# Performance work log

Hardware: AMD Instinct MI355X
Metric: run time of the kernel (lower is better)

The kernel has to match this reference:

```python
import jax, jax.numpy as jnp
import numpy as np

N_NODES = 8192
N_EDGES = 65536
NB = 10            # number_of_basis
MID = 32           # middle_layer_size
MAX_R = 10.0       # max_radius
NZ, NM = 48, 16    # z / mol embedding sizes -> 64x0e node input
IN_S = NZ + NM     # 64 scalars
H_S, H_V = 32, 8   # hidden irreps 32x0e + 8x1o (dim 56)
O_S = 16           # output irreps 16x0e
W0N = IN_S * H_S + IN_S * H_V                                  # 2560
W1N = H_S*H_S + H_V*H_S + H_S*H_V + H_V*H_V + H_V*H_V          # 1664
W2N = H_S*O_S + H_V*O_S                                        # 640
H_DIM = H_S + 3 * H_V                                          # 56


def _fcnet(e, W1, W2):
    # e3nn FullyConnectedNet([NB, MID, numel], silu): fan-in normalized linears
    h = jax.nn.silu(e @ W1 / np.sqrt(W1.shape[0]))
    return h @ W2 / np.sqrt(W2.shape[0])


def _ln(x, g, b):
    m = jnp.mean(x, -1, keepdims=True)
    v = jnp.var(x, -1, keepdims=True)
    return (x - m) * jax.lax.rsqrt(v + 1e-5) * g + b


def _sus(t):
    # smooth compact-support bump helper: exp(-1/t) for t>0 else 0
    return jnp.where(t > 0, jnp.exp(-1.0 / jnp.where(t > 0, t, 1.0)), 0.0)


def _forward(pos, Ez, Em,
             b0_W1, b0_W2, b0_g, b0_b,
             b1_W1, b1_W2, b1_g, b1_b,
             b2_W1, b2_W2, b2_g, b2_b,
             z, mol_id, edge_src, edge_dst):
    N = pos.shape[0]
    E = edge_src.shape[0]
    avg = E / N  # avg_num_neighbors (static)

    # node embedding: 64x0e
    x = jnp.concatenate([Ez[z], Em[mol_id]], axis=-1)          # [N, 64]

    vec = pos[edge_dst] - pos[edge_src]                        # [E, 3]
    length = jnp.linalg.norm(vec, axis=1)                      # [E]

    # soft_one_hot_linspace(basis='smooth_finite', cutoff=True) * sqrt(NB)
    vals = jnp.linspace(0.0, MAX_R, NB + 2)[1:-1]
    step = MAX_R / (NB + 1)
    u = (length[:, None] - vals) / step
    emb = (1.14136 * np.exp(2.0)) * _sus(u + 1.0) * _sus(1.0 - u)
    emb = emb * np.sqrt(NB)                                    # [E, NB]

    # spherical harmonics lmax=1, normalize=True, 'component' norm
    nrm = vec / jnp.maximum(length, 1e-9)[:, None]
    sh_v = np.sqrt(3.0) * nrm                                  # [E, 3]  (l=1; l=0 comp == 1)

    # ---- interaction block 0: 64x0e -> 32x0e + 8x1o ----
    w = _fcnet(emb, b0_W1, b0_W2)                              # [E, 2560]
    w00 = w[:, :IN_S * H_S].reshape(E, IN_S, H_S)
    w01 = w[:, IN_S * H_S:].reshape(E, IN_S, H_V)
    xe = x[edge_src]                                           # [E, 64]
    es = jnp.einsum('eu,euw->ew', xe, w00) / np.sqrt(IN_S)
    ev = jnp.einsum('eu,euw,ei->ewi', xe, w01, sh_v) / np.sqrt(IN_S)
    msg = jnp.concatenate([es, ev.reshape(E, 3 * H_V)], -1)    # [E, 56]
    x = _ln(jax.ops.segment_sum(msg, edge_dst, num_segments=N) / np.sqrt(avg), b0_g, b0_b)

    # ---- interaction block 1: 32x0e+8x1o -> 32x0e+8x1o ----
    w = _fcnet(emb, b1_W1, b1_W2)                              # [E, 1664]
    o = 0
    w_ss  = w[:, o:o + H_S*H_S].reshape(E, H_S, H_S); o += H_S*H_S
    w_vvs = w[:, o:o + H_V*H_S].reshape(E, H_V, H_S); o += H_V*H_S
    w_sv  = w[:, o:o + H_S*H_V].reshape(E, H_S, H_V); o += H_S*H_V
    w_vs  = w[:, o:o + H_V*H_V].reshape(E, H_V, H_V); o += H_V*H_V
    w_vvv = w[:, o:o + H_V*H_V].reshape(E, H_V, H_V)
    xs = x[:, :H_S][edge_src]                                  # [E, 32]
    xv = x[:, H_S:].reshape(N, H_V, 3)[edge_src]               # [E, 8, 3]
    dot = jnp.einsum('eui,ei->eu', xv, sh_v) / np.sqrt(3.0)    # 1o x 1o -> 0e CG
    crs = jnp.cross(xv, sh_v[:, None, :]) / np.sqrt(2.0)       # 1o x 1o -> 1o CG
    es = (jnp.einsum('eu,euw->ew', xs, w_ss) / np.sqrt(H_S)
          + jnp.einsum('eu,euw->ew', dot, w_vvs) / np.sqrt(H_V)) / np.sqrt(2.0)
    ev = (jnp.einsum('eu,euw,ei->ewi', xs, w_sv, sh_v) / np.sqrt(H_S)
          + jnp.einsum('eui,euw->ewi', xv, w_vs) / np.sqrt(H_V)
          + jnp.einsum('eui,euw->ewi', crs, w_vvv) / np.sqrt(H_V)) / np.sqrt(3.0)
    msg = jnp.concatenate([es, ev.reshape(E, 3 * H_V)], -1)
    x = _ln(jax.ops.segment_sum(msg, edge_dst, num_segments=N) / np.sqrt(avg), b1_g, b1_b)

    # ---- interaction block 2: 32x0e+8x1o -> 16x0e ----
    w = _fcnet(emb, b2_W1, b2_W2)                              # [E, 640]
    w_ss  = w[:, :H_S * O_S].reshape(E, H_S, O_S)
    w_vvs = w[:, H_S * O_S:].reshape(E, H_V, O_S)
    xs = x[:, :H_S][edge_src]
    xv = x[:, H_S:].reshape(N, H_V, 3)[edge_src]
    dot = jnp.einsum('eui,ei->eu', xv, sh_v) / np.sqrt(3.0)
    es = (jnp.einsum('eu,euw->ew', xs, w_ss) / np.sqrt(H_S)
          + jnp.einsum('eu,euw->ew', dot, w_vvs) / np.sqrt(H_V)) / np.sqrt(2.0)
    x = _ln(jax.ops.segment_sum(es, edge_dst, num_segments=N) / np.sqrt(avg), b2_g, b2_b)
    return x                                                   # [N, 16]


def setup_inputs():
    key = jax.random.key(0)
    ks = jax.random.split(key, 16)
    edge_src = jax.random.randint(ks[3], (N_EDGES,), 0, N_NODES)
    # exclude self-loops (radius_graph never returns them)
    edge_dst = (edge_src + 1 + jax.random.randint(ks[4], (N_EDGES,), 0, N_NODES - 1)) % N_NODES
    return {
        'pos': jax.random.uniform(ks[0], (N_NODES, 3), jnp.float32) * 8.0,
        'z': jax.random.randint(ks[1], (N_NODES,), 0, 100),
        'mol_id': jax.random.randint(ks[2], (N_NODES,), 0, 2),
        'edge_src': edge_src,
        'edge_dst': edge_dst,
        'Ez': jax.random.normal(ks[5], (100, NZ), jnp.float32),
        'Em': jax.random.normal(ks[6], (2, NM), jnp.float32),
        'b0_W1': jax.random.normal(ks[7], (NB, MID), jnp.float32),
        'b0_W2': jax.random.normal(ks[8], (MID, W0N), jnp.float32),
        'b0_g': jnp.ones((H_DIM,), jnp.float32),
        'b0_b': jnp.zeros((H_DIM,), jnp.float32),
        'b1_W1': jax.random.normal(ks[9], (NB, MID), jnp.float32),
        'b1_W2': jax.random.normal(ks[10], (MID, W1N), jnp.float32),
        'b1_g': jnp.ones((H_DIM,), jnp.float32),
        'b1_b': jnp.zeros((H_DIM,), jnp.float32),
        'b2_W1': jax.random.normal(ks[11], (NB, MID), jnp.float32),
        'b2_W2': jax.random.normal(ks[12], (MID, W2N), jnp.float32),
        'b2_g': jnp.ones((O_S,), jnp.float32),
        'b2_b': jnp.zeros((O_S,), jnp.float32),
    }


def reference(pos, z, mol_id, edge_src, edge_dst, Ez, Em,
              b0_W1, b0_W2, b0_g, b0_b,
              b1_W1, b1_W2, b1_g, b1_b,
              b2_W1, b2_W2, b2_g, b2_b):
    return _forward(pos, Ez, Em,
                    b0_W1, b0_W2, b0_g, b0_b,
                    b1_W1, b1_W2, b1_g, b1_b,
                    b2_W1, b2_W2, b2_g, b2_b,
                    z, mol_id, edge_src, edge_dst)
```

## Files before the change

### kernel.cpp

```cpp
#include <hip/hip_runtime.h>

#define NNODES 8192
#define NEDGES 65536

#define K_PACK   0.02209708691f
#define K_P1SV   0.01804219593f
#define K_VVS    0.04419417382f
#define K_VS     0.03608439182f
#define K_VVV    0.02551551815f
#define K_DOT    0.57735026919f
#define K_PRELN  0.35355339059f
#define C_EMB    8.4335730689f

typedef unsigned int uint32;
typedef unsigned short ushort16;
typedef __attribute__((ext_vector_type(8))) short short8;
typedef __attribute__((ext_vector_type(4))) float floatx4;

__device__ __forceinline__ float siluf(float x) { return x / (1.0f + __expf(-x)); }
__device__ __forceinline__ float susf(float t) { return t > 0.0f ? __expf(-1.0f / t) : 0.0f; }
__device__ __forceinline__ ushort16 f2bf(float f) {
  uint32 u = __float_as_uint(f);
  return (ushort16)((u + 0x7fffu + ((u >> 16) & 1u)) >> 16);
}
__device__ __forceinline__ float bflo(uint32 v) { return __uint_as_float(v << 16); }
__device__ __forceinline__ float bfhi(uint32 v) { return __uint_as_float(v & 0xffff0000u); }

__device__ __forceinline__ void mlp32(const float* __restrict__ W, const float emb[10],
                                      float* __restrict__ H) {
#pragma unroll
  for (int m = 0; m < 32; ++m) {
    float t = 0.f;
#pragma unroll
    for (int k = 0; k < 10; ++k) t += emb[k] * W[k * 32 + m];
    H[m] = siluf(t);
  }
}

__global__ __launch_bounds__(256) void k_prep(
    const float* __restrict__ pos, const int* __restrict__ z, const int* __restrict__ mol,
    const int* __restrict__ esrc, const int* __restrict__ edst,
    const float* __restrict__ Ez, const float* __restrict__ Em,
    const float* __restrict__ W10, const float* __restrict__ W11, const float* __restrict__ W12,
    const float* __restrict__ W20, const float* __restrict__ W21, const float* __restrict__ W22,
    int* __restrict__ combo, ushort16* __restrict__ X0cb, float* __restrict__ sh,
    float* __restrict__ h0, float* __restrict__ h1, float* __restrict__ h2,
    ushort16* __restrict__ h1b, ushort16* __restrict__ h2b,
    ushort16* __restrict__ Bp0, ushort16* __restrict__ Bp1, ushort16* __restrict__ Bp2,
    ushort16* __restrict__ Bpw1, ushort16* __restrict__ Bpw2, int* __restrict__ deg) {
  int idx = blockIdx.x * 256 + threadIdx.x;
  if (idx < NEDGES) {
    int e = idx;
    int s = esrc[e], d = edst[e];
    atomicAdd(&deg[d], 1);
    float vx = pos[d * 3 + 0] - pos[s * 3 + 0];
    float vy = pos[d * 3 + 1] - pos[s * 3 + 1];
    float vz = pos[d * 3 + 2] - pos[s * 3 + 2];
    float len = sqrtf(vx * vx + vy * vy + vz * vz);
    float inv = 1.7320508076f / fmaxf(len, 1e-9f);
    sh[e * 3 + 0] = vx * inv; sh[e * 3 + 1] = vy * inv; sh[e * 3 + 2] = vz * inv;
    float emb[10];
#pragma unroll
    for (int k = 0; k < 10; ++k) {
      float u = len * 1.1f - (float)(k + 1);
      emb[k] = C_EMB * susf(u + 1.0f) * susf(1.0f - u);
    }
    float H[32];
    mlp32(W10, emb, H);
#pragma unroll
    for (int m = 0; m < 32; ++m) h0[(size_t)e * 32 + m] = H[m];
    mlp32(W11, emb, H);
#pragma unroll
    for (int m = 0; m < 32; ++m) {
      h1[(size_t)e * 32 + m] = H[m];
      h1b[(size_t)e * 32 + m] = f2bf(H[m]);
    }
    mlp32(W12, emb, H);
#pragma unroll
    for (int m = 0; m < 32; ++m) {
      h2[(size_t)e * 32 + m] = H[m];
      h2b[(size_t)e * 32 + m] = f2bf(H[m]);
    }
    return;
  }
  idx -= NEDGES;
  if (idx < NNODES) { combo[idx] = z[idx] * 2 + mol[idx]; return; }
  idx -= NNODES;
  if (idx < 16384) {
    int c = idx >> 6, j = idx & 63;
    float v = 0.f;
    if (c < 200) {
      int zz = c >> 1, mm = c & 1;
      v = (j < 48) ? Ez[zz * 48 + j] : Em[mm * 16 + (j - 48)];
    }
    X0cb[idx] = f2bf(v);
    return;
  }
  idx -= 16384;
  if (idx < 81920) {
    int tile = idx >> 10; int r = idx & 1023;
    int kh = r >> 9; int rr = r & 511;
    int lane = rr >> 3, j = rr & 7;
    int k = kh * 32 + (lane >> 4) * 8 + j;
    int n = tile * 16 + (lane & 15);
    int c = n >> 5, m = n & 31;
    int col = (c < 32) ? (k * 32 + c) : (2048 + k * 8 + (c - 32));
    Bp0[idx] = f2bf(W20[m * 2560 + col] * K_PACK);
    return;
  }
  idx -= 81920;
  if (idx < 40960) {
    int tile = idx >> 9; int rr = idx & 511;
    int lane = rr >> 3, j = rr & 7;
    int k = (lane >> 4) * 8 + j;
    int n = tile * 16 + (lane & 15);
    int c = n >> 5, m = n & 31;
    float v = (c < 32) ? W21[m * 1664 + k * 32 + c] * K_PACK
                       : W21[m * 1664 + 1280 + k * 8 + (c - 32)] * K_P1SV;
    Bp1[idx] = f2bf(v);
    return;
  }
  idx -= 40960;
  if (idx < 16384) {
    int tile = idx >> 9; int rr = idx & 511;
    int lane = rr >> 3, j = rr & 7;
    int k = (lane >> 4) * 8 + j;
    int n = tile * 16 + (lane & 15);
    int c = n >> 5, m = n & 31;
    Bp2[idx] = f2bf(W22[m * 640 + k * 16 + c] * K_PACK);
    return;
  }
  idx -= 16384;
  if (idx < 12288) {
    int tile = idx >> 9; int rr = idx & 511;
    int lane = rr >> 3, j = rr & 7;
    int m = (lane >> 4) * 8 + j;
    int c = tile * 16 + (lane & 15);
    float v;
    if (c < 256) {
      int u = c >> 5, w = c & 31;
      v = W21[m * 1664 + 1024 + u * 32 + w] * K_VVS;
    } else {
      int r2 = c - 256; int t = r2 & 1; int l2 = r2 >> 1;
      int u = l2 >> 3, vv = l2 & 7;
      v = (t == 0) ? W21[m * 1664 + 1536 + u * 8 + vv] * K_VS
                   : W21[m * 1664 + 1600 + u * 8 + vv] * K_VVV;
    }
    Bpw1[idx] = f2bf(v);
    return;
  }
  idx -= 12288;
  {
    int tile = idx >> 9; int rr = idx & 511;
    int lane = rr >> 3, j = rr & 7;
    int m = (lane >> 4) * 8 + j;
    int c = tile * 16 + (lane & 15);
    int t = c & 1; int l2 = c >> 1;
    int u = l2 >> 3, wh = l2 & 7;
    Bpw2[idx] = f2bf(W22[m * 640 + 512 + u * 16 + wh * 2 + t] * K_VVS);
  }
}

__global__ __launch_bounds__(256) void k_scan(const int* __restrict__ deg,
                                              int* __restrict__ rowptr) {
  __shared__ int sums[256];
  int t = threadIdx.x;
  int base = t * 32;
  int local[32];
  int s = 0;
#pragma unroll
  for (int i = 0; i < 32; ++i) { local[i] = s; s += deg[base + i]; }
  sums[t] = s;
  __syncthreads();
  for (int off = 1; off < 256; off <<= 1) {
    int v = (t >= off) ? sums[t - off] : 0;
    __syncthreads();
    sums[t] += v;
    __syncthreads();
  }
  int prev = (t == 0) ? 0 : sums[t - 1];
#pragma unroll
  for (int i = 0; i < 32; ++i) rowptr[base + i] = prev + local[i];
  if (t == 255) rowptr[NNODES] = sums[255];
}

__global__ __launch_bounds__(256) void k_fill(const int* __restrict__ edst,
                                              const int* __restrict__ rowptr,
                                              int* __restrict__ fill, int* __restrict__ eidx) {
  int e = blockIdx.x * 256 + threadIdx.x;
  if (e >= NEDGES) return;
  int d = edst[e];
  int p = atomicAdd(&fill[d], 1);
  eidx[rowptr[d] + p] = e;
}

__global__ __launch_bounds__(256) void k_gemm_mfma(
    const ushort16* __restrict__ A, const ushort16* __restrict__ Bp, ushort16* __restrict__ C,
    int N, int K) {
  int wave = threadIdx.x >> 6, lane = threadIdx.x & 63;
  int m0 = blockIdx.x * 64 + wave * 16;
  int n0 = blockIdx.y * 64;
  int row = lane & 15, q = lane >> 4;
  int nkh = K >> 5;
  floatx4 acc[4];
  floatx4 zero = {0.f, 0.f, 0.f, 0.f};
#pragma unroll
  for (int t = 0; t < 4; ++t) acc[t] = zero;
  for (int kh = 0; kh < nkh; ++kh) {
    short8 a = *reinterpret_cast<const short8*>(A + (size_t)(m0 + row) * K + kh * 32 + q * 8);
#pragma unroll
    for (int t = 0; t < 4; ++t) {
      int T = (n0 >> 4) + t;
      short8 b = *reinterpret_cast<const short8*>(Bp + ((size_t)T * nkh + kh) * 512 + lane * 8);
      acc[t] = __builtin_amdgcn_mfma_f32_16x16x32_bf16(a, b, acc[t], 0, 0, 0);
    }
  }
  int colb = n0 + row;
#pragma unroll
  for (int t = 0; t < 4; ++t)
#pragma unroll
    for (int r = 0; r < 4; ++r)
      C[(size_t)(m0 + q * 4 + r) * N + colb + t * 16] = f2bf(acc[t][r]);
}

__global__ __launch_bounds__(256) void k_msg0(
    const int* __restrict__ rowmap, const int* __restrict__ esrc,
    const float* __restrict__ sh, const float* __restrict__ h,
    const ushort16* __restrict__ Pb, float* __restrict__ msg) {
  int e = __builtin_amdgcn_readfirstlane(blockIdx.x * 4 + (threadIdx.x >> 6));
  int lane = threadIdx.x & 63;
  int s = esrc[e];
  int row = rowmap[s];
  float sh0 = sh[e * 3 + 0], sh1 = sh[e * 3 + 1], sh2 = sh[e * 3 + 2];
  int c; float mult;
  if (lane < 32) { c = lane; mult = 1.0f; }
  else if (lane < 56) {
    int l = lane - 32; int v = l / 3; int i = l - v * 3;
    c = 32 + v;
    mult = (i == 0) ? sh0 : (i == 1 ? sh1 : sh2);
  } else { c = 0; mult = 0.0f; }
  const float* hp = h + (size_t)e * 32;
  const uint4* Pp = reinterpret_cast<const uint4*>(Pb + (size_t)row * 1280 + c * 32);
  float a = 0.f;
#pragma unroll
  for (int qq = 0; qq < 4; ++qq) {
    uint4 pv = Pp[qq];
    const float* hq = hp + qq * 8;
    a += bflo(pv.x) * hq[0] + bfhi(pv.x) * hq[1];
    a += bflo(pv.y) * hq[2] + bfhi(pv.y) * hq[3];
    a += bflo(pv.z) * hq[4] + bfhi(pv.z) * hq[5];
    a += bflo(pv.w) * hq[6] + bfhi(pv.w) * hq[7];
  }
  if (lane < 56) msg[(size_t)e * 56 + lane] = a * mult;
}

__global__ __launch_bounds__(256) void k_msg1(
    const int* __restrict__ esrc, const float* __restrict__ sh, const float* __restrict__ h,
    const ushort16* __restrict__ Pb, const float* __restrict__ xv,
    const ushort16* __restrict__ Wedge, float* __restrict__ msg) {
  __shared__ float vbuf[4][56];
  int w = threadIdx.x >> 6;
  int e = __builtin_amdgcn_readfirstlane(blockIdx.x * 4 + w);
  int lane = threadIdx.x & 63;
  int s = esrc[e];
  float sh0 = sh[e * 3 + 0], sh1 = sh[e * 3 + 1], sh2 = sh[e * 3 + 2];
  int u = lane >> 3;
  const float* xvp = xv + (size_t)s * 24 + u * 3;
  float x0 = xvp[0], x1 = xvp[1], x2 = xvp[2];
  float du = K_DOT * (x0 * sh0 + x1 * sh1 + x2 * sh2);
  float cr0 = x1 * sh2 - x2 * sh1;
  float cr1 = x2 * sh0 - x0 * sh2;
  float cr2 = x0 * sh1 - x1 * sh0;
  const ushort16* wp = Wedge + (size_t)e * 384;
  uint2 wv = *reinterpret_cast<const uint2*>(wp + lane * 4);
  uint32 wsv = *reinterpret_cast<const uint32*>(wp + 256 + lane * 2);
  float b0 = du * bflo(wv.x), b1 = du * bfhi(wv.x);
  float b2 = du * bflo(wv.y), b3 = du * bfhi(wv.y);
  float avs = bflo(wsv), avv = bfhi(wsv);
  float e0v = x0 * avs + cr0 * avv;
  float e1v = x1 * avs + cr1 * avv;
  float e2v = x2 * avs + cr2 * avv;
#pragma unroll
  for (int off = 8; off < 64; off <<= 1) {
    b0 += __shfl_xor(b0, off, 64); b1 += __shfl_xor(b1, off, 64);
    b2 += __shfl_xor(b2, off, 64); b3 += __shfl_xor(b3, off, 64);
    e0v += __shfl_xor(e0v, off, 64); e1v += __shfl_xor(e1v, off, 64);
    e2v += __shfl_xor(e2v, off, 64);
  }
  if (lane < 8) {
    vbuf[w][lane * 4 + 0] = b0; vbuf[w][lane * 4 + 1] = b1;
    vbuf[w][lane * 4 + 2] = b2; vbuf[w][lane * 4 + 3] = b3;
    vbuf[w][32 + lane * 3 + 0] = e0v;
    vbuf[w][32 + lane * 3 + 1] = e1v;
    vbuf[w][32 + lane * 3 + 2] = e2v;
  }
  int c; float mult;
  if (lane < 32) { c = lane; mult = 1.0f; }
  else if (lane < 56) {
    int l = lane - 32; int v = l / 3; int i = l - v * 3;
    c = 32 + v;
    mult = (i == 0) ? sh0 : (i == 1 ? sh1 : sh2);
  } else { c = 0; mult = 0.0f; }
  const float* hp = h + (size_t)e * 32;
  const uint4* Pp = reinterpret_cast<const uint4*>(Pb + (size_t)s * 1280 + c * 32);
  float a = 0.f;
#pragma unroll
  for (int qq = 0; qq < 4; ++qq) {
    uint4 pv = Pp[qq];
    const float* hq = hp + qq * 8;
    a += bflo(pv.x) * hq[0] + bfhi(pv.x) * hq[1];
    a += bflo(pv.y) * hq[2] + bfhi(pv.y) * hq[3];
    a += bflo(pv.z) * hq[4] + bfhi(pv.z) * hq[5];
    a += bflo(pv.w) * hq[6] + bfhi(pv.w) * hq[7];
  }
  __syncthreads();
  if (lane < 56) msg[(size_t)e * 56 + lane] = a * mult + vbuf[w][lane];
}

__global__ __launch_bounds__(256) void k_msg2(
    const int* __restrict__ esrc, const float* __restrict__ sh, const float* __restrict__ h,
    const ushort16* __restrict__ Pb, const float* __restrict__ xv,
    const ushort16* __restrict__ Wedge, float* __restrict__ msg) {
  __shared__ float vbuf[4][16];
  int w = threadIdx.x >> 6;
  int e = __builtin_amdgcn_readfirstlane(blockIdx.x * 4 + w);
  int lane = threadIdx.x & 63;
  int s = esrc[e];
  float sh0 = sh[e * 3 + 0], sh1 = sh[e * 3 + 1], sh2 = sh[e * 3 + 2];
  int u = lane >> 3;
  const float* xvp = xv + (size_t)s * 24 + u * 3;
  float du = K_DOT * (xvp[0] * sh0 + xvp[1] * sh1 + xvp[2] * sh2);
  uint32 w2 = *reinterpret_cast<const uint32*>(Wedge + (size_t)e * 128 + lane * 2);
  float c0 = du * bflo(w2), c1 = du * bfhi(w2);
#pragma unroll
  for (int off = 8; off < 64; off <<= 1) {
    c0 += __shfl_xor(c0, off, 64); c1 += __shfl_xor(c1, off, 64);
  }
  if (lane < 8) { vbuf[w][lane * 2 + 0] = c0; vbuf[w][lane * 2 + 1] = c1; }
  int q = lane >> 4, wc = lane & 15;
  const float* hq = h + (size_t)e * 32 + q * 8;
  uint4 pv = reinterpret_cast<const uint4*>(Pb + (size_t)s * 512 + wc * 32)[q];
  float a = bflo(pv.x) * hq[0] + bfhi(pv.x) * hq[1]
          + bflo(pv.y) * hq[2] + bfhi(pv.y) * hq[3]
          + bflo(pv.z) * hq[4] + bfhi(pv.z) * hq[5]
          + bflo(pv.w) * hq[6] + bfhi(pv.w) * hq[7];
  a += __shfl_xor(a, 16, 64);
  a += __shfl_xor(a, 32, 64);
  __syncthreads();
  if (lane < 16) msg[(size_t)e * 16 + lane] = a + vbuf[w][lane];
}

__global__ __launch_bounds__(256) void k_gather_ln(
    const int* __restrict__ rowptr, const int* __restrict__ eidx,
    const float* __restrict__ msg, int D,
    const float* __restrict__ g, const float* __restrict__ b,
    ushort16* __restrict__ xsb, float* __restrict__ xvf, float* __restrict__ outf) {
  int n = __builtin_amdgcn_readfirstlane(blockIdx.x * 4 + (threadIdx.x >> 6));
  int lane = threadIdx.x & 63;
  int r0 = rowptr[n], r1 = rowptr[n + 1];
  float v = 0.f;
  for (int j = r0; j < r1; ++j) {
    int e = eidx[j];
    if (lane < D) v += msg[(size_t)e * D + lane];
  }
  v *= K_PRELN;
  if (lane >= D) v = 0.f;
  float sm = v, sq = v * v;
#pragma unroll
  for (int off = 32; off > 0; off >>= 1) {
    sm += __shfl_xor(sm, off, 64);
    sq += __shfl_xor(sq, off, 64);
  }
  float invD = 1.0f / (float)D;
  float mean = sm * invD;
  float var = sq * invD - mean * mean;
  float rs = rsqrtf(var + 1e-5f);
  float r = (v - mean) * rs * g[lane < D ? lane : 0] + b[lane < D ? lane : 0];
  if (outf) {
    if (lane < D) outf[(size_t)n * D + lane] = r;
  } else {
    if (lane < 32) xsb[(size_t)n * 32 + lane] = f2bf(r);
    else if (lane < 56) xvf[(size_t)n * 24 + lane - 32] = r;
  }
}

extern "C" void kernel_launch(void* const* d_in, const int* in_sizes, int n_in,
                              void* d_out, int out_size, void* d_ws, size_t ws_size,
                              hipStream_t stream) {
  const float* pos = (const float*)d_in[0];
  const int* z = (const int*)d_in[1];
  const int* mol = (const int*)d_in[2];
  const int* esrc = (const int*)d_in[3];
  const int* edst = (const int*)d_in[4];
  const float* Ez = (const float*)d_in[5];
  const float* Em = (const float*)d_in[6];
  const float* b0W1 = (const float*)d_in[7];
  const float* b0W2 = (const float*)d_in[8];
  const float* b0g = (const float*)d_in[9];
  const float* b0b = (const float*)d_in[10];
  const float* b1W1 = (const float*)d_in[11];
  const float* b1W2 = (const float*)d_in[12];
  const float* b1g = (const float*)d_in[13];
  const float* b1b = (const float*)d_in[14];
  const float* b2W1 = (const float*)d_in[15];
  const float* b2W2 = (const float*)d_in[16];
  const float* b2g = (const float*)d_in[17];
  const float* b2b = (const float*)d_in[18];
  float* out = (float*)d_out;

  float* ws = (float*)d_ws;
  size_t o = 0;
  int* combo = (int*)(ws + o); o += NNODES;
  int* deg = (int*)(ws + o); o += NNODES;
  int* fill = (int*)(ws + o); o += NNODES;
  int* rowptr = (int*)(ws + o); o += NNODES + 8;
  int* eidx = (int*)(ws + o); o += NEDGES;
  ushort16* X0cb = (ushort16*)(ws + o); o += 8192;
  ushort16* xs1b = (ushort16*)(ws + o); o += 131072;
  float* xv1 = ws + o; o += (size_t)NNODES * 24;
  float* h0 = ws + o; o += (size_t)NEDGES * 32;
  float* h1 = ws + o; o += (size_t)NEDGES * 32;
  float* h2 = ws + o; o += (size_t)NEDGES * 32;
  float* shb = ws + o; o += (size_t)NEDGES * 3;
  ushort16* Bp0 = (ushort16*)(ws + o); o += 40960;
  ushort16* Bp1 = (ushort16*)(ws + o); o += 20480;
  ushort16* Bp2 = (ushort16*)(ws + o); o += 8192;
  ushort16* Bpw1 = (ushort16*)(ws + o); o += 6144;
  ushort16* Bpw2 = (ushort16*)(ws + o); o += 2048;
  ushort16* h1b = (ushort16*)(ws + o); o += (size_t)NEDGES * 16;
  ushort16* h2b = (ushort16*)(ws + o); o += (size_t)NEDGES * 16;
  ushort16* Wedge1 = (ushort16*)(ws + o); o += (size_t)NEDGES * 192;
  ushort16* P12 = (ushort16*)(ws + o); o += (size_t)NNODES * 640;
  float* msg56 = ws + o; o += (size_t)NEDGES * 56;

  ushort16* P0c = P12;
  ushort16* xs2b = xs1b;
  float* xv2 = xv1;
  ushort16* Wedge2 = Wedge1;
  float* msg16 = msg56;

  hipMemsetAsync(deg, 0, 2 * NNODES * sizeof(int), stream);

  k_prep<<<960, 256, 0, stream>>>(pos, z, mol, esrc, edst, Ez, Em,
                                  b0W1, b1W1, b2W1, b0W2, b1W2, b2W2,
                                  combo, X0cb, shb, h0, h1, h2, h1b, h2b,
                                  Bp0, Bp1, Bp2, Bpw1, Bpw2, deg);
  k_scan<<<1, 256, 0, stream>>>(deg, rowptr);
  k_fill<<<256, 256, 0, stream>>>(edst, rowptr, fill, eidx);

  k_gemm_mfma<<<dim3(4, 20), 256, 0, stream>>>(X0cb, Bp0, P0c, 1280, 64);
  k_gemm_mfma<<<dim3(1024, 6), 256, 0, stream>>>(h1b, Bpw1, Wedge1, 384, 32);
  k_msg0<<<16384, 256, 0, stream>>>(combo, esrc, shb, h0, P0c, msg56);
  k_gather_ln<<<2048, 256, 0, stream>>>(rowptr, eidx, msg56, 56, b0g, b0b, xs1b, xv1, nullptr);

  k_gemm_mfma<<<dim3(128, 20), 256, 0, stream>>>(xs1b, Bp1, P12, 1280, 32);
  k_msg1<<<16384, 256, 0, stream>>>(esrc, shb, h1, P12, xv1, Wedge1, msg56);
  k_gather_ln<<<2048, 256, 0, stream>>>(rowptr, eidx, msg56, 56, b1g, b1b, xs2b, xv2, nullptr);

  k_gemm_mfma<<<dim3(1024, 2), 256, 0, stream>>>(h2b, Bpw2, Wedge2, 128, 32);
  k_gemm_mfma<<<dim3(128, 8), 256, 0, stream>>>(xs2b, Bp2, P12, 512, 32);
  k_msg2<<<16384, 256, 0, stream>>>(esrc, shb, h2, P12, xv2, Wedge2, msg16);
  k_gather_ln<<<2048, 256, 0, stream>>>(rowptr, eidx, msg16, 16, b2g, b2b, nullptr, nullptr, out);
}
```

Measured before the change: 254.2 us.

## Store edge MLP hidden as bf16 only and batch three GEMMs into one launch

The edge radial-MLP hidden activations are now written only as packed bf16, and the fp32 copies go away. The message kernels read them with 16-byte vector loads, which cuts k_prep store traffic and halves the hidden-vector reads in msg0/msg1/msg2. Three independent GEMMs (the Wedge1 and Wedge2 edge-weight GEMMs and the P0 node GEMM) are merged into a single launch with a block-index dispatcher. Wedge2 gets its own buffer so it can be computed early. The cost is extra workspace and a small precision loss from using bf16 hidden values in the fp32-P dot products.

Result: no change. 256.5 us (+0.9%).

```diff
diff --git a/kernel.cpp b/kernel.cpp
--- a/kernel.cpp
+++ b/kernel.cpp
@@ -44,8 +44,7 @@
     const float* __restrict__ W10, const float* __restrict__ W11, const float* __restrict__ W12,
     const float* __restrict__ W20, const float* __restrict__ W21, const float* __restrict__ W22,
     int* __restrict__ combo, ushort16* __restrict__ X0cb, float* __restrict__ sh,
-    float* __restrict__ h0, float* __restrict__ h1, float* __restrict__ h2,
-    ushort16* __restrict__ h1b, ushort16* __restrict__ h2b,
+    ushort16* __restrict__ h0b, ushort16* __restrict__ h1b, ushort16* __restrict__ h2b,
     ushort16* __restrict__ Bp0, ushort16* __restrict__ Bp1, ushort16* __restrict__ Bp2,
     ushort16* __restrict__ Bpw1, ushort16* __restrict__ Bpw2, int* __restrict__ deg) {
   int idx = blockIdx.x * 256 + threadIdx.x;
@@ -66,21 +65,22 @@
       emb[k] = C_EMB * susf(u + 1.0f) * susf(1.0f - u);
     }
     float H[32];
+    uint32* hp;
     mlp32(W10, emb, H);
-#pragma unroll
-    for (int m = 0; m < 32; ++m) h0[(size_t)e * 32 + m] = H[m];
+    hp = (uint32*)(h0b + (size_t)e * 32);
+#pragma unroll
+    for (int m = 0; m < 16; ++m)
+      hp[m] = (uint32)f2bf(H[2 * m]) | ((uint32)f2bf(H[2 * m + 1]) << 16);
     mlp32(W11, emb, H);
-#pragma unroll
-    for (int m = 0; m < 32; ++m) {
-      h1[(size_t)e * 32 + m] = H[m];
-      h1b[(size_t)e * 32 + m] = f2bf(H[m]);
-    }
+    hp = (uint32*)(h1b + (size_t)e * 32);
+#pragma unroll
+    for (int m = 0; m < 16; ++m)
+      hp[m] = (uint32)f2bf(H[2 * m]) | ((uint32)f2bf(H[2 * m + 1]) << 16);
     mlp32(W12, emb, H);
-#pragma unroll
-    for (int m = 0; m < 32; ++m) {
-      h2[(size_t)e * 32 + m] = H[m];
-      h2b[(size_t)e * 32 + m] = f2bf(H[m]);
-    }
+    hp = (uint32*)(h2b + (size_t)e * 32);
+#pragma unroll
+    for (int m = 0; m < 16; ++m)
+      hp[m] = (uint32)f2bf(H[2 * m]) | ((uint32)f2bf(H[2 * m + 1]) << 16);
     return;
   }
   idx -= NEDGES;
@@ -194,12 +194,11 @@
   eidx[rowptr[d] + p] = e;
 }
 
-__global__ __launch_bounds__(256) void k_gemm_mfma(
+__device__ __forceinline__ void gemm_tile(
     const ushort16* __restrict__ A, const ushort16* __restrict__ Bp, ushort16* __restrict__ C,
-    int N, int K) {
-  int wave = threadIdx.x >> 6, lane = threadIdx.x & 63;
-  int m0 = blockIdx.x * 64 + wave * 16;
-  int n0 = blockIdx.y * 64;
+    int N, int K, int bx, int by, int wave, int lane) {
+  int m0 = bx * 64 + wave * 16;
+  int n0 = by * 64;
   int row = lane & 15, q = lane >> 4;
   int nkh = K >> 5;
   floatx4 acc[4];
@@ -223,9 +222,35 @@
       C[(size_t)(m0 + q * 4 + r) * N + colb + t * 16] = f2bf(acc[t][r]);
 }
 
+__global__ __launch_bounds__(256) void k_gemm_mfma(
+    const ushort16* __restrict__ A, const ushort16* __restrict__ Bp, ushort16* __restrict__ C,
+    int N, int K) {
+  gemm_tile(A, Bp, C, N, K, blockIdx.x, blockIdx.y, threadIdx.x >> 6, threadIdx.x & 63);
+}
+
+__global__ __launch_bounds__(256) void k_gemm3(
+    const ushort16* __restrict__ A0, const ushort16* __restrict__ B0, ushort16* __restrict__ C0,
+    int N0, int K0, int nbx0, int nb0,
+    const ushort16* __restrict__ A1, const ushort16* __restrict__ B1, ushort16* __restrict__ C1,
+    int N1, int K1, int nbx1, int nb1,
+    const ushort16* __restrict__ A2, const ushort16* __restrict__ B2, ushort16* __restrict__ C2,
+    int N2, int K2, int nbx2) {
+  int b = blockIdx.x;
+  int wave = threadIdx.x >> 6, lane = threadIdx.x & 63;
+  if (b < nb0) {
+    gemm_tile(A0, B0, C0, N0, K0, b % nbx0, b / nbx0, wave, lane);
+  } else if (b < nb0 + nb1) {
+    b -= nb0;
+    gemm_tile(A1, B1, C1, N1, K1, b % nbx1, b / nbx1, wave, lane);
+  } else {
+    b -= nb0 + nb1;
+    gemm_tile(A2, B2, C2, N2, K2, b % nbx2, b / nbx2, wave, lane);
+  }
+}
+
 __global__ __launch_bounds__(256) void k_msg0(
     const int* __restrict__ rowmap, const int* __restrict__ esrc,
-    const float* __restrict__ sh, const float* __restrict__ h,
+    const float* __restrict__ sh, const ushort16* __restrict__ hb,
     const ushort16* __restrict__ Pb, float* __restrict__ msg) {
   int e = __builtin_amdgcn_readfirstlane(blockIdx.x * 4 + (threadIdx.x >> 6));
   int lane = threadIdx.x & 63;
@@ -239,23 +264,23 @@
     c = 32 + v;
     mult = (i == 0) ? sh0 : (i == 1 ? sh1 : sh2);
   } else { c = 0; mult = 0.0f; }
-  const float* hp = h + (size_t)e * 32;
+  const uint4* Hp = reinterpret_cast<const uint4*>(hb + (size_t)e * 32);
   const uint4* Pp = reinterpret_cast<const uint4*>(Pb + (size_t)row * 1280 + c * 32);
   float a = 0.f;
 #pragma unroll
   for (int qq = 0; qq < 4; ++qq) {
     uint4 pv = Pp[qq];
-    const float* hq = hp + qq * 8;
-    a += bflo(pv.x) * hq[0] + bfhi(pv.x) * hq[1];
-    a += bflo(pv.y) * hq[2] + bfhi(pv.y) * hq[3];
-    a += bflo(pv.z) * hq[4] + bfhi(pv.z) * hq[5];
-    a += bflo(pv.w) * hq[6] + bfhi(pv.w) * hq[7];
+    uint4 hv = Hp[qq];
+    a += bflo(pv.x) * bflo(hv.x) + bfhi(pv.x) * bfhi(hv.x);
+    a += bflo(pv.y) * bflo(hv.y) + bfhi(pv.y) * bfhi(hv.y);
+    a += bflo(pv.z) * bflo(hv.z) + bfhi(pv.z) * bfhi(hv.z);
+    a += bflo(pv.w) * bflo(hv.w) + bfhi(pv.w) * bfhi(hv.w);
   }
   if (lane < 56) msg[(size_t)e * 56 + lane] = a * mult;
 }
 
 __global__ __launch_bounds__(256) void k_msg1(
-    const int* __restrict__ esrc, const float* __restrict__ sh, const float* __restrict__ h,
+    const int* __restrict__ esrc, const float* __restrict__ sh, const ushort16* __restrict__ hb,
     const ushort16* __restrict__ Pb, const float* __restrict__ xv,
     const ushort16* __restrict__ Wedge, float* __restrict__ msg) {
   __shared__ float vbuf[4][56];
@@ -301,24 +326,24 @@
     c = 32 + v;
     mult = (i == 0) ? sh0 : (i == 1 ? sh1 : sh2);
   } else { c = 0; mult = 0.0f; }
-  const float* hp = h + (size_t)e * 32;
+  const uint4* Hp = reinterpret_cast<const uint4*>(hb + (size_t)e * 32);
   const uint4* Pp = reinterpret_cast<const uint4*>(Pb + (size_t)s * 1280 + c * 32);
   float a = 0.f;
 #pragma unroll
   for (int qq = 0; qq < 4; ++qq) {
     uint4 pv = Pp[qq];
-    const float* hq = hp + qq * 8;
-    a += bflo(pv.x) * hq[0] + bfhi(pv.x) * hq[1];
-    a += bflo(pv.y) * hq[2] + bfhi(pv.y) * hq[3];
-    a += bflo(pv.z) * hq[4] + bfhi(pv.z) * hq[5];
-    a += bflo(pv.w) * hq[6] + bfhi(pv.w) * hq[7];
+    uint4 hv = Hp[qq];
+    a += bflo(pv.x) * bflo(hv.x) + bfhi(pv.x) * bfhi(hv.x);
+    a += bflo(pv.y) * bflo(hv.y) + bfhi(pv.y) * bfhi(hv.y);
+    a += bflo(pv.z) * bflo(hv.z) + bfhi(pv.z) * bfhi(hv.z);
+    a += bflo(pv.w) * bflo(hv.w) + bfhi(pv.w) * bfhi(hv.w);
   }
   __syncthreads();
   if (lane < 56) msg[(size_t)e * 56 + lane] = a * mult + vbuf[w][lane];
 }
 
 __global__ __launch_bounds__(256) void k_msg2(
-    const int* __restrict__ esrc, const float* __restrict__ sh, const float* __restrict__ h,
+    const int* __restrict__ esrc, const float* __restrict__ sh, const ushort16* __restrict__ hb,
     const ushort16* __restrict__ Pb, const float* __restrict__ xv,
     const ushort16* __restrict__ Wedge, float* __restrict__ msg) {
   __shared__ float vbuf[4][16];
@@ -338,12 +363,12 @@
   }
   if (lane < 8) { vbuf[w][lane * 2 + 0] = c0; vbuf[w][lane * 2 + 1] = c1; }
   int q = lane >> 4, wc = lane & 15;
-  const float* hq = h + (size_t)e * 32 + q * 8;
+  uint4 hv = reinterpret_cast<const uint4*>(hb + (size_t)e * 32)[q];
   uint4 pv = reinterpret_cast<const uint4*>(Pb + (size_t)s * 512 + wc * 32)[q];
-  float a = bflo(pv.x) * hq[0] + bfhi(pv.x) * hq[1]
-          + bflo(pv.y) * hq[2] + bfhi(pv.y) * hq[3]
-          + bflo(pv.z) * hq[4] + bfhi(pv.z) * hq[5]
-          + bflo(pv.w) * hq[6] + bfhi(pv.w) * hq[7];
+  float a = bflo(pv.x) * bflo(hv.x) + bfhi(pv.x) * bfhi(hv.x)
+          + bflo(pv.y) * bflo(hv.y) + bfhi(pv.y) * bfhi(hv.y)
+          + bflo(pv.z) * bflo(hv.z) + bfhi(pv.z) * bfhi(hv.z)
+          + bflo(pv.w) * bflo(hv.w) + bfhi(pv.w) * bfhi(hv.w);
   a += __shfl_xor(a, 16, 64);
   a += __shfl_xor(a, 32, 64);
   __syncthreads();
@@ -418,47 +443,46 @@
   ushort16* X0cb = (ushort16*)(ws + o); o += 8192;
   ushort16* xs1b = (ushort16*)(ws + o); o += 131072;
   float* xv1 = ws + o; o += (size_t)NNODES * 24;
-  float* h0 = ws + o; o += (size_t)NEDGES * 32;
-  float* h1 = ws + o; o += (size_t)NEDGES * 32;
-  float* h2 = ws + o; o += (size_t)NEDGES * 32;
+  ushort16* h0b = (ushort16*)(ws + o); o += (size_t)NEDGES * 16;
+  ushort16* h1b = (ushort16*)(ws + o); o += (size_t)NEDGES * 16;
+  ushort16* h2b = (ushort16*)(ws + o); o += (size_t)NEDGES * 16;
   float* shb = ws + o; o += (size_t)NEDGES * 3;
   ushort16* Bp0 = (ushort16*)(ws + o); o += 40960;
   ushort16* Bp1 = (ushort16*)(ws + o); o += 20480;
   ushort16* Bp2 = (ushort16*)(ws + o); o += 8192;
   ushort16* Bpw1 = (ushort16*)(ws + o); o += 6144;
   ushort16* Bpw2 = (ushort16*)(ws + o); o += 2048;
-  ushort16* h1b = (ushort16*)(ws + o); o += (size_t)NEDGES * 16;
-  ushort16* h2b = (ushort16*)(ws + o); o += (size_t)NEDGES * 16;
   ushort16* Wedge1 = (ushort16*)(ws + o); o += (size_t)NEDGES * 192;
+  ushort16* Wedge2 = (ushort16*)(ws + o); o += (size_t)NEDGES * 64;
   ushort16* P12 = (ushort16*)(ws + o); o += (size_t)NNODES * 640;
   float* msg56 = ws + o; o += (size_t)NEDGES * 56;
 
   ushort16* P0c = P12;
   ushort16* xs2b = xs1b;
   float* xv2 = xv1;
-  ushort16* Wedge2 = Wedge1;
   float* msg16 = msg56;
 
   hipMemsetAsync(deg, 0, 2 * NNODES * sizeof(int), stream);
 
   k_prep<<<960, 256, 0, stream>>>(pos, z, mol, esrc, edst, Ez, Em,
                                   b0W1, b1W1, b2W1, b0W2, b1W2, b2W2,
-                                  combo, X0cb, shb, h0, h1, h2, h1b, h2b,
+                                  combo, X0cb, shb, h0b, h1b, h2b,
                                   Bp0, Bp1, Bp2, Bpw1, Bpw2, deg);
   k_scan<<<1, 256, 0, stream>>>(deg, rowptr);
   k_fill<<<256, 256, 0, stream>>>(edst, rowptr, fill, eidx);
 
-  k_gemm_mfma<<<dim3(4, 20), 256, 0, stream>>>(X0cb, Bp0, P0c, 1280, 64);
-  k_gemm_mfma<<<dim3(1024, 6), 256, 0, stream>>>(h1b, Bpw1, Wedge1, 384, 32);
-  k_msg0<<<16384, 256, 0, stream>>>(combo, esrc, shb, h0, P0c, msg56);
+  k_gemm3<<<8272, 256, 0, stream>>>(h1b, Bpw1, Wedge1, 384, 32, 1024, 6144,
+                                    h2b, Bpw2, Wedge2, 128, 32, 1024, 2048,
+                                    X0cb, Bp0, P0c, 1280, 64, 4);
+
+  k_msg0<<<16384, 256, 0, stream>>>(combo, esrc, shb, h0b, P0c, msg56);
   k_gather_ln<<<2048, 256, 0, stream>>>(rowptr, eidx, msg56, 56, b0g, b0b, xs1b, xv1, nullptr);
 
   k_gemm_mfma<<<dim3(128, 20), 256, 0, stream>>>(xs1b, Bp1, P12, 1280, 32);
-  k_msg1<<<16384, 256, 0, stream>>>(esrc, shb, h1, P12, xv1, Wedge1, msg56);
+  k_msg1<<<16384, 256, 0, stream>>>(esrc, shb, h1b, P12, xv1, Wedge1, msg56);
   k_gather_ln<<<2048, 256, 0, stream>>>(rowptr, eidx, msg56, 56, b1g, b1b, xs2b, xv2, nullptr);
 
-  k_gemm_mfma<<<dim3(1024, 2), 256, 0, stream>>>(h2b, Bpw2, Wedge2, 128, 32);
   k_gemm_mfma<<<dim3(128, 8), 256, 0, stream>>>(xs2b, Bp2, P12, 512, 32);
-  k_msg2<<<16384, 256, 0, stream>>>(esrc, shb, h2, P12, xv2, Wedge2, msg16);
+  k_msg2<<<16384, 256, 0, stream>>>(esrc, shb, h2b, P12, xv2, Wedge2, msg16);
   k_gather_ln<<<2048, 256, 0, stream>>>(rowptr, eidx, msg16, 16, b2g, b2b, nullptr, nullptr, out);
 }
```
